# Kernel optimization log

Measured on AMD Instinct MI355X. Metric: run time of the kernel, lower is better.

The kernel has to match this reference:

```python
import jax, jax.numpy as jnp
import numpy as np

K = 8192
D = 512


def setup_inputs() -> dict:
    key = jax.random.key(0)
    k1, k2 = jax.random.split(key)
    x = jax.random.normal(k1, (32, 512, D), dtype=jnp.float32)
    # nn.Embedding weight init: uniform(-1/k, 1/k)
    codebook = jax.random.uniform(k2, (K, D), dtype=jnp.float32,
                                  minval=-1.0 / K, maxval=1.0 / K)
    return {"x": x, "codebook": codebook}


def reference(x, codebook):
    # flatten to [N, D]
    z_e = x.reshape(-1, x.shape[-1])
    # squared L2 distances: ||z||^2 - 2 z c^T + ||c||^2  -> [N, K]
    dists = (jnp.sum(z_e * z_e, axis=1, keepdims=True)
             - 2.0 * jnp.einsum('nd,kd->nk', z_e, codebook)
             + jnp.sum(codebook * codebook, axis=1)[None, :])
    indices = jnp.argmin(dists, axis=1)  # [N]
    z_q = codebook[indices]              # [N, D] gather
    # straight-through estimator: forward z_q, grad passes to z_e
    z_q_st = z_e + jax.lax.stop_gradient(z_q - z_e)
    # vq loss pulls codebook toward (detached) encoder outputs
    vq_loss = jnp.mean((z_q - jax.lax.stop_gradient(z_e)) ** 2)
    # commitment loss pulls encoder outputs toward (detached) codes
    commit_loss = jnp.mean((z_e - jax.lax.stop_gradient(z_q)) ** 2)
    z_q_out = z_q_st.reshape(x.shape)
    idx_out = indices.reshape(x.shape[:-1])
    return z_q_out, vq_loss, commit_loss, idx_out
```

## Files before the change

### kernel.cpp

```cpp
#include <hip/hip_runtime.h>

#define K_CODES 8192
#define D_DIM   512
#define N_ROWS  16384
#define NSPLIT  32
#define CAP     8
#define T2      2.0e-4f
#define LIST_CAP 32768

typedef __attribute__((ext_vector_type(8))) short bf16x8;
typedef __attribute__((ext_vector_type(4))) float f32x4;
typedef unsigned char uchar;
typedef unsigned short ushort;
typedef unsigned long long u64;

__device__ __forceinline__ unsigned fkey(float f) {
    unsigned b = __float_as_uint(f);
    return (b & 0x80000000u) ? ~b : (b | 0x80000000u);
}
__device__ __forceinline__ float finv(unsigned k) {
    return __uint_as_float((k & 0x80000000u) ? (k & 0x7fffffffu) : ~k);
}

__device__ __forceinline__ unsigned pk_bf16(float a, float b) {
    unsigned ua = __float_as_uint(a), ub = __float_as_uint(b);
    ua = (ua + 0x7fffu + ((ua >> 16) & 1u)) >> 16;
    ub = (ub + 0x7fffu + ((ub >> 16) & 1u)) & 0xffff0000u;
    return ua | ub;
}

__device__ __forceinline__ void gload_lds16(const void* g, void* l) {
    __builtin_amdgcn_global_load_lds(
        (const __attribute__((address_space(1))) unsigned int*)g,
        (__attribute__((address_space(3))) unsigned int*)l, 16, 0, 0);
}

__global__ void vq_prepass(const float* __restrict__ x, const float* __restrict__ cb,
                           unsigned* __restrict__ xb, unsigned* __restrict__ cbb,
                           float* __restrict__ sn, u64* __restrict__ keys,
                           int* __restrict__ count) {
    const int bid = blockIdx.x;
    const int t = threadIdx.x;
    if (bid < 6144) {
        const size_t gid = (size_t)bid * 256 + t;
        const size_t nx = (size_t)N_ROWS * D_DIM / 8;
        if (gid < nx) {
            const float4 f0 = ((const float4*)x)[gid * 2];
            const float4 f1 = ((const float4*)x)[gid * 2 + 1];
            ((uint4*)xb)[gid] = make_uint4(pk_bf16(f0.x, f0.y), pk_bf16(f0.z, f0.w),
                                           pk_bf16(f1.x, f1.y), pk_bf16(f1.z, f1.w));
        } else {
            const size_t g = gid - nx;
            const float4 f0 = ((const float4*)cb)[g * 2];
            const float4 f1 = ((const float4*)cb)[g * 2 + 1];
            ((uint4*)cbb)[g] = make_uint4(pk_bf16(f0.x, f0.y), pk_bf16(f0.z, f0.w),
                                          pk_bf16(f1.x, f1.y), pk_bf16(f1.z, f1.w));
        }
    } else {
        const int base = (bid - 6144) * 8;
        if (bid == 6144 && t == 0) *count = 0;
        if (t < 8) keys[base + t] = ~0ull;
        const int wave = t >> 6, lane = t & 63;
        const int row = base + wave * 2 + (lane >> 5);
        const int l = lane & 31, b = l >> 3, j = l & 7;
        const float* a = x + (size_t)row * D_DIM + b * 128 + j;
        float r = __fmul_rn(a[0], a[0]);
#pragma unroll
        for (int i = 1; i < 16; ++i) {
            const float v = a[i * 8];
            r = __fadd_rn(r, __fmul_rn(v, v));
        }
        r = __fadd_rn(r, __shfl_xor(r, 1));
        r = __fadd_rn(r, __shfl_xor(r, 2));
        r = __fadd_rn(r, __shfl_xor(r, 4));
        r = __fadd_rn(r, __shfl_xor(r, 8));
        r = __fadd_rn(r, __shfl_xor(r, 16));
        if (l == 0) sn[row] = r;
    }
}

__global__ __launch_bounds__(256)
void vq_sn(const float* __restrict__ x, float* __restrict__ sn,
           u64* __restrict__ keys, int* __restrict__ count) {
    const int t = threadIdx.x;
    const int base = blockIdx.x * 8;
    if (blockIdx.x == 0 && t == 0) *count = 0;
    if (t < 8) keys[base + t] = ~0ull;
    const int wave = t >> 6, lane = t & 63;
    const int row = base + wave * 2 + (lane >> 5);
    const int l = lane & 31, b = l >> 3, j = l & 7;
    const float* a = x + (size_t)row * D_DIM + b * 128 + j;
    float r = __fmul_rn(a[0], a[0]);
#pragma unroll
    for (int i = 1; i < 16; ++i) {
        const float v = a[i * 8];
        r = __fadd_rn(r, __fmul_rn(v, v));
    }
    r = __fadd_rn(r, __shfl_xor(r, 1));
    r = __fadd_rn(r, __shfl_xor(r, 2));
    r = __fadd_rn(r, __shfl_xor(r, 4));
    r = __fadd_rn(r, __shfl_xor(r, 8));
    r = __fadd_rn(r, __shfl_xor(r, 16));
    if (l == 0) sn[row] = r;
}

template<bool PRE>
__global__ __launch_bounds__(256, 2)
void vq_screen2(const float* __restrict__ x, const float* __restrict__ cb,
                const ushort* __restrict__ xb, const ushort* __restrict__ cbb,
                float* __restrict__ g_dmax, uchar* __restrict__ g_cnt,
                uchar* __restrict__ g_cand) {
    __shared__ ushort Ash[128 * 32];
    __shared__ ushort Bsh[256 * 32];
    __shared__ unsigned vkey[128];
    __shared__ int ccnt[128];
    __shared__ uchar clist[128][CAP];

    const int t    = threadIdx.x;
    const int w    = t >> 6, lane = t & 63;
    const int fr   = lane & 15;
    const int quad = lane >> 4;
    const int wr   = (w & 1) * 64;
    const int wc   = (w >> 1) * 128;
    const int row0  = blockIdx.y * 128;
    const int kbase = blockIdx.x * 256;

    if (t < 128) { vkey[t] = 0u; ccnt[t] = 0; }

    int aoff[4], boff[8];
#pragma unroll
    for (int i = 0; i < 4; ++i) {
        const int rw = wr + i * 16 + fr;
        aoff[i] = rw * 32 + ((quad ^ (rw >> 1)) & 3) * 8;
    }
#pragma unroll
    for (int j = 0; j < 8; ++j) {
        const int rw = wc + j * 16 + fr;
        boff[j] = rw * 32 + ((quad ^ (rw >> 1)) & 3) * 8;
    }

    f32x4 acc[4][8];
#pragma unroll
    for (int i = 0; i < 4; ++i)
#pragma unroll
        for (int j = 0; j < 8; ++j) acc[i][j] = (f32x4)0.0f;

    if (PRE) {
        const int la = lane >> 2;
        const int p  = lane & 3;
        const char* srcA0; const char* srcA1;
        const char* srcB0; const char* srcB1; const char* srcB2; const char* srcB3;
        ushort* dstA0; ushort* dstA1;
        ushort* dstB0; ushort* dstB1; ushort* dstB2; ushort* dstB3;
        {
            const int ia0 = w * 2 + 0, rA0 = ia0 * 16 + la;
            const int ia1 = w * 2 + 1, rA1 = ia1 * 16 + la;
            srcA0 = (const char*)xb + (size_t)(row0 + rA0) * 1024 + ((p ^ ((rA0 >> 1) & 3)) * 16);
            srcA1 = (const char*)xb + (size_t)(row0 + rA1) * 1024 + ((p ^ ((rA1 >> 1) & 3)) * 16);
            dstA0 = &Ash[ia0 * 512];
            dstA1 = &Ash[ia1 * 512];
            const int ib0 = w * 4 + 0, rB0 = ib0 * 16 + la;
            const int ib1 = w * 4 + 1, rB1 = ib1 * 16 + la;
            const int ib2 = w * 4 + 2, rB2 = ib2 * 16 + la;
            const int ib3 = w * 4 + 3, rB3 = ib3 * 16 + la;
            srcB0 = (const char*)cbb + (size_t)(kbase + rB0) * 1024 + ((p ^ ((rB0 >> 1) & 3)) * 16);
            srcB1 = (const char*)cbb + (size_t)(kbase + rB1) * 1024 + ((p ^ ((rB1 >> 1) & 3)) * 16);
            srcB2 = (const char*)cbb + (size_t)(kbase + rB2) * 1024 + ((p ^ ((rB2 >> 1) & 3)) * 16);
            srcB3 = (const char*)cbb + (size_t)(kbase + rB3) * 1024 + ((p ^ ((rB3 >> 1) & 3)) * 16);
            dstB0 = &Bsh[ib0 * 512];
            dstB1 = &Bsh[ib1 * 512];
            dstB2 = &Bsh[ib2 * 512];
            dstB3 = &Bsh[ib3 * 512];
        }
        for (int dc = 0; dc < 16; ++dc) {
            __syncthreads();
            gload_lds16(srcA0, dstA0);
            gload_lds16(srcA1, dstA1);
            gload_lds16(srcB0, dstB0);
            gload_lds16(srcB1, dstB1);
            gload_lds16(srcB2, dstB2);
            gload_lds16(srcB3, dstB3);
            srcA0 += 64; srcA1 += 64;
            srcB0 += 64; srcB1 += 64; srcB2 += 64; srcB3 += 64;
            __syncthreads();
            bf16x8 af[4], bfv[8];
#pragma unroll
            for (int i = 0; i < 4; ++i) af[i] = *(const bf16x8*)&Ash[aoff[i]];
#pragma unroll
            for (int j = 0; j < 8; ++j) bfv[j] = *(const bf16x8*)&Bsh[boff[j]];
#pragma unroll
            for (int i = 0; i < 4; ++i)
#pragma unroll
                for (int j = 0; j < 8; ++j)
                    acc[i][j] = __builtin_amdgcn_mfma_f32_16x16x32_bf16(af[i], bfv[j], acc[i][j], 0, 0, 0);
        }
    } else {
        const int r = t >> 1, h = t & 1;
        const int sA = (r >> 1) & 3;
        const int ca0 = (2 * h) ^ sA;
        ushort* awp0 = &Ash[r * 32 + ca0 * 8];
        ushort* awp1 = &Ash[r * 32 + (ca0 ^ 1) * 8];
        const int sB = (t >> 1) & 3;
        ushort* bwp0 = &Bsh[t * 32 + (0 ^ sB) * 8];
        ushort* bwp1 = &Bsh[t * 32 + (1 ^ sB) * 8];
        ushort* bwp2 = &Bsh[t * 32 + (2 ^ sB) * 8];
        ushort* bwp3 = &Bsh[t * 32 + (3 ^ sB) * 8];
        const char* gA = (const char*)(x  + (size_t)(row0 + r) * D_DIM + h * 16);
        const char* gB = (const char*)(cb + (size_t)(kbase + t) * D_DIM);
        for (int dc = 0; dc < 16; ++dc) {
            const float4* fa = (const float4*)(gA + dc * 128);
            float4 f0 = fa[0], f1 = fa[1], f2 = fa[2], f3 = fa[3];
            uint4 a0 = make_uint4(pk_bf16(f0.x, f0.y), pk_bf16(f0.z, f0.w),
                                  pk_bf16(f1.x, f1.y), pk_bf16(f1.z, f1.w));
            uint4 a1 = make_uint4(pk_bf16(f2.x, f2.y), pk_bf16(f2.z, f2.w),
                                  pk_bf16(f3.x, f3.y), pk_bf16(f3.z, f3.w));
            const float4* fb = (const float4*)(gB + dc * 128);
            float4 g0 = fb[0], g1 = fb[1], g2 = fb[2], g3 = fb[3];
            float4 g4 = fb[4], g5 = fb[5], g6 = fb[6], g7 = fb[7];
            uint4 b0 = make_uint4(pk_bf16(g0.x, g0.y), pk_bf16(g0.z, g0.w),
                                  pk_bf16(g1.x, g1.y), pk_bf16(g1.z, g1.w));
            uint4 b1 = make_uint4(pk_bf16(g2.x, g2.y), pk_bf16(g2.z, g2.w),
                                  pk_bf16(g3.x, g3.y), pk_bf16(g3.z, g3.w));
            uint4 b2 = make_uint4(pk_bf16(g4.x, g4.y), pk_bf16(g4.z, g4.w),
                                  pk_bf16(g5.x, g5.y), pk_bf16(g5.z, g5.w));
            uint4 b3 = make_uint4(pk_bf16(g6.x, g6.y), pk_bf16(g6.z, g6.w),
                                  pk_bf16(g7.x, g7.y), pk_bf16(g7.z, g7.w));
            __syncthreads();
            *(uint4*)awp0 = a0; *(uint4*)awp1 = a1;
            *(uint4*)bwp0 = b0; *(uint4*)bwp1 = b1;
            *(uint4*)bwp2 = b2; *(uint4*)bwp3 = b3;
            __syncthreads();
            bf16x8 af[4], bfv[8];
#pragma unroll
            for (int i = 0; i < 4; ++i) af[i] = *(const bf16x8*)&Ash[aoff[i]];
#pragma unroll
            for (int j = 0; j < 8; ++j) bfv[j] = *(const bf16x8*)&Bsh[boff[j]];
#pragma unroll
            for (int i = 0; i < 4; ++i)
#pragma unroll
                for (int j = 0; j < 8; ++j)
                    acc[i][j] = __builtin_amdgcn_mfma_f32_16x16x32_bf16(af[i], bfv[j], acc[i][j], 0, 0, 0);
        }
    }

    __syncthreads();
#pragma unroll
    for (int i = 0; i < 4; ++i)
#pragma unroll
        for (int rg = 0; rg < 4; ++rg) {
            float m = acc[i][0][rg];
#pragma unroll
            for (int j = 1; j < 8; ++j) m = fmaxf(m, acc[i][j][rg]);
            m = fmaxf(m, __shfl_xor(m, 1));
            m = fmaxf(m, __shfl_xor(m, 2));
            m = fmaxf(m, __shfl_xor(m, 4));
            m = fmaxf(m, __shfl_xor(m, 8));
            if (fr == 0) atomicMax(&vkey[wr + i * 16 + quad * 4 + rg], fkey(m));
        }
    __syncthreads();
#pragma unroll
    for (int i = 0; i < 4; ++i)
#pragma unroll
        for (int rg = 0; rg < 4; ++rg) {
            const int row = wr + i * 16 + quad * 4 + rg;
            const float thr = finv(vkey[row]) - T2;
#pragma unroll
            for (int j = 0; j < 8; ++j) {
                if (acc[i][j][rg] >= thr) {
                    int p = atomicAdd(&ccnt[row], 1);
                    if (p < CAP) clist[row][p] = (uchar)(wc + j * 16 + fr);
                }
            }
        }
    __syncthreads();
    if (t < 128) {
        const size_t o = (size_t)(row0 + t) * NSPLIT + blockIdx.x;
        g_dmax[o] = finv(vkey[t]);
        int c = ccnt[t];
        g_cnt[o] = (uchar)(c > 255 ? 255 : c);
        ((uint2*)g_cand)[o] = *(const uint2*)clist[t];
    }
}

__global__ __launch_bounds__(256)
void vq_build(const float* __restrict__ g_dmax, const uchar* __restrict__ g_cnt,
              const uchar* __restrict__ g_cand, int2* __restrict__ list,
              int* __restrict__ count, float* __restrict__ idx_f) {
    const int row = blockIdx.x * blockDim.x + threadIdx.x;
    const int lane = threadIdx.x & 63;
    const float* dm = g_dmax + (size_t)row * NSPLIT;
    float g = dm[0];
#pragma unroll
    for (int s = 1; s < NSPLIT; ++s) g = fmaxf(g, dm[s]);
    const float thr = g - T2;

    int tot = 0, first = -1;
    for (int s = 0; s < NSPLIT; ++s) {
        if (dm[s] < thr) continue;
        const size_t o = (size_t)row * NSPLIT + s;
        const int c = g_cnt[o];
        tot += (c > CAP) ? 256 : c;
        if (first < 0) first = s * 256 + g_cand[o * CAP];
    }
    idx_f[row] = (float)first;

    const int need = (tot > 1) ? tot : 0;
    int scan = need;
#pragma unroll
    for (int d = 1; d < 64; d <<= 1) {
        const int v = __shfl_up(scan, d, 64);
        if (lane >= d) scan += v;
    }
    const int wtot = __shfl(scan, 63, 64);
    int base = 0;
    if (lane == 63 && wtot > 0) base = atomicAdd(count, wtot);
    base = __shfl(base, 63, 64);
    if (need == 0) return;
    int pos = base + scan - need;

    for (int s = 0; s < NSPLIT; ++s) {
        if (dm[s] < thr) continue;
        const size_t o = (size_t)row * NSPLIT + s;
        const int c = g_cnt[o];
        if (c > CAP) {
            for (int u = 0; u < 256; ++u, ++pos)
                if (pos < LIST_CAP) list[pos] = make_int2(row, s * 256 + u);
        } else {
            for (int u = 0; u < c; ++u, ++pos)
                if (pos < LIST_CAP) list[pos] = make_int2(row, s * 256 + g_cand[o * CAP + u]);
        }
    }
}

__device__ __forceinline__ float np_einsum_dot(const float* __restrict__ a,
                                               const float* __restrict__ b) {
    float S0 = 0.f, S1 = 0.f, S2 = 0.f, S3 = 0.f;
    for (int i = 0; i < D_DIM; i += 16) {
        S0 = __fadd_rn(S0, __fmul_rn(a[i + 12], b[i + 12]));
        S1 = __fadd_rn(S1, __fmul_rn(a[i + 13], b[i + 13]));
        S2 = __fadd_rn(S2, __fmul_rn(a[i + 14], b[i + 14]));
        S3 = __fadd_rn(S3, __fmul_rn(a[i + 15], b[i + 15]));
        S0 = __fadd_rn(S0, __fmul_rn(a[i +  8], b[i +  8]));
        S1 = __fadd_rn(S1, __fmul_rn(a[i +  9], b[i +  9]));
        S2 = __fadd_rn(S2, __fmul_rn(a[i + 10], b[i + 10]));
        S3 = __fadd_rn(S3, __fmul_rn(a[i + 11], b[i + 11]));
        S0 = __fadd_rn(S0, __fmul_rn(a[i +  4], b[i +  4]));
        S1 = __fadd_rn(S1, __fmul_rn(a[i +  5], b[i +  5]));
        S2 = __fadd_rn(S2, __fmul_rn(a[i +  6], b[i +  6]));
        S3 = __fadd_rn(S3, __fmul_rn(a[i +  7], b[i +  7]));
        S0 = __fadd_rn(S0, __fmul_rn(a[i +  0], b[i +  0]));
        S1 = __fadd_rn(S1, __fmul_rn(a[i +  1], b[i +  1]));
        S2 = __fadd_rn(S2, __fmul_rn(a[i +  2], b[i +  2]));
        S3 = __fadd_rn(S3, __fmul_rn(a[i +  3], b[i +  3]));
    }
    return __fadd_rn(__fadd_rn(S0, S1), __fadd_rn(S2, S3));
}

__global__ __launch_bounds__(256)
void vq_replay(const float* __restrict__ x, const float* __restrict__ cb,
               const float* __restrict__ sn, const int2* __restrict__ list,
               const int* __restrict__ count, u64* __restrict__ keys) {
    const int i = blockIdx.x * blockDim.x + threadIdx.x;
    int n = *count; if (n > LIST_CAP) n = LIST_CAP;
    if (i >= n) return;
    const int2 e = list[i];
    const float* zr = x + (size_t)e.x * D_DIM;
    const float d = __fadd_rn(sn[e.x],
                              __fmul_rn(-2.0f, np_einsum_dot(zr, cb + (size_t)e.y * D_DIM)));
    const u64 key = ((u64)fkey(d) << 32) | (unsigned)e.y;
    atomicMin(&keys[e.x], key);
}

__global__ void vq_gather_kernel(const float* __restrict__ x,
                                 const float* __restrict__ cb,
                                 const u64* __restrict__ keys,
                                 float* __restrict__ idx_f,
                                 float* __restrict__ zq_out,
                                 double* __restrict__ psum) {
    const int row = blockIdx.x;
    const int t   = threadIdx.x;
    const u64 ky = keys[row];
    const int k = (ky != ~0ull) ? (int)(ky & 0xffffffffu) : (int)idx_f[row];
    const float4 c  = ((const float4*)(cb + (size_t)k   * D_DIM))[t];
    const float4 xv = ((const float4*)(x  + (size_t)row * D_DIM))[t];
    float4 o;
    o.x = __fadd_rn(xv.x, __fsub_rn(c.x, xv.x));
    o.y = __fadd_rn(xv.y, __fsub_rn(c.y, xv.y));
    o.z = __fadd_rn(xv.z, __fsub_rn(c.z, xv.z));
    o.w = __fadd_rn(xv.w, __fsub_rn(c.w, xv.w));
    ((float4*)(zq_out + (size_t)row * D_DIM))[t] = o;
    const double d0 = (double)c.x - (double)xv.x;
    const double d1 = (double)c.y - (double)xv.y;
    const double d2 = (double)c.z - (double)xv.z;
    const double d3 = (double)c.w - (double)xv.w;
    double s = d0 * d0 + d1 * d1 + d2 * d2 + d3 * d3;
#pragma unroll
    for (int off = 32; off > 0; off >>= 1) s += __shfl_xor(s, off, 64);
    __shared__ double red[2];
    if ((t & 63) == 0) red[t >> 6] = s;
    __syncthreads();
    if (t == 0) {
        psum[row] = red[0] + red[1];
        idx_f[row] = (float)k;
    }
}

__global__ void vq_finalize2(const double* __restrict__ psum,
                             float* __restrict__ losses) {
    __shared__ double red[4];
    const int t = threadIdx.x;
    double s = 0.0;
    for (int i = t; i < N_ROWS; i += 256) s += psum[i];
#pragma unroll
    for (int off = 32; off > 0; off >>= 1) s += __shfl_xor(s, off, 64);
    if ((t & 63) == 0) red[t >> 6] = s;
    __syncthreads();
    if (t == 0) {
        const double tot = red[0] + red[1] + red[2] + red[3];
        const float l = (float)(tot / (double)((size_t)N_ROWS * D_DIM));
        losses[0] = l;
        losses[1] = l;
    }
}

extern "C" void kernel_launch(void* const* d_in, const int* in_sizes, int n_in,
                              void* d_out, int out_size, void* d_ws, size_t ws_size,
                              hipStream_t stream) {
    const float* x  = (const float*)d_in[0];
    const float* cb = (const float*)d_in[1];
    float* out    = (float*)d_out;
    float* zq     = out;
    float* losses = out + (size_t)N_ROWS * D_DIM;
    float* idx_f  = losses + 2;
    char* ws = (char*)d_ws;

    const bool pre = (ws_size >= ((size_t)32 << 20));
    char* base = pre ? (ws + ((size_t)24 << 20)) : ws;

    float*  g_dmax = (float*)(base);
    uchar*  g_cnt  = (uchar*)(base + (2048u << 10));
    uchar*  g_cand = (uchar*)(base + (2560u << 10));
    float*  sn     = (float*)(base + (6656u << 10));
    u64*    keys   = (u64*)  (base + (6720u << 10));
    int2*   list   = (int2*) (base + (6848u << 10));
    int*    count  = (int*)  (base + (7104u << 10));
    double* psum   = (double*)(base + (7168u << 10));

    if (pre) {
        ushort* xb  = (ushort*)ws;
        ushort* cbb = (ushort*)(ws + ((size_t)16 << 20));
        hipLaunchKernelGGL(vq_prepass, dim3(8192), dim3(256), 0, stream,
                           x, cb, (unsigned*)xb, (unsigned*)cbb, sn, keys, count);
        hipLaunchKernelGGL((vq_screen2<true>), dim3(K_CODES / 256, N_ROWS / 128), dim3(256), 0, stream,
                           x, cb, xb, cbb, g_dmax, g_cnt, g_cand);
    } else {
        hipLaunchKernelGGL(vq_sn, dim3(N_ROWS / 8), dim3(256), 0, stream,
                           x, sn, keys, count);
        hipLaunchKernelGGL((vq_screen2<false>), dim3(K_CODES / 256, N_ROWS / 128), dim3(256), 0, stream,
                           x, cb, (const ushort*)nullptr, (const ushort*)nullptr,
                           g_dmax, g_cnt, g_cand);
    }
    hipLaunchKernelGGL(vq_build, dim3(N_ROWS / 256), dim3(256), 0, stream,
                       g_dmax, g_cnt, g_cand, list, count, idx_f);
    hipLaunchKernelGGL(vq_replay, dim3(LIST_CAP / 256), dim3(256), 0, stream,
                       x, cb, sn, list, count, keys);
    hipLaunchKernelGGL(vq_gather_kernel, dim3(N_ROWS), dim3(128), 0, stream,
                       x, cb, keys, idx_f, zq, psum);
    hipLaunchKernelGGL(vq_finalize2, dim3(1), dim3(256), 0, stream,
                       psum, losses);
}
```

Baseline: 384.7 us.

## Double-buffer LDS tiles in screening GEMM to overlap global loads with MFMA

```diff
diff --git a/kernel.cpp b/kernel.cpp
--- a/kernel.cpp
+++ b/kernel.cpp
@@ -110,8 +110,8 @@
                 const ushort* __restrict__ xb, const ushort* __restrict__ cbb,
                 float* __restrict__ g_dmax, uchar* __restrict__ g_cnt,
                 uchar* __restrict__ g_cand) {
-    __shared__ ushort Ash[128 * 32];
-    __shared__ ushort Bsh[256 * 32];
+    __shared__ ushort Ash[2][128 * 32];
+    __shared__ ushort Bsh[2][256 * 32];
     __shared__ unsigned vkey[128];
     __shared__ int ccnt[128];
     __shared__ uchar clist[128][CAP];
@@ -148,63 +148,63 @@
     if (PRE) {
         const int la = lane >> 2;
         const int p  = lane & 3;
-        const char* srcA0; const char* srcA1;
-        const char* srcB0; const char* srcB1; const char* srcB2; const char* srcB3;
-        ushort* dstA0; ushort* dstA1;
-        ushort* dstB0; ushort* dstB1; ushort* dstB2; ushort* dstB3;
-        {
-            const int ia0 = w * 2 + 0, rA0 = ia0 * 16 + la;
-            const int ia1 = w * 2 + 1, rA1 = ia1 * 16 + la;
-            srcA0 = (const char*)xb + (size_t)(row0 + rA0) * 1024 + ((p ^ ((rA0 >> 1) & 3)) * 16);
-            srcA1 = (const char*)xb + (size_t)(row0 + rA1) * 1024 + ((p ^ ((rA1 >> 1) & 3)) * 16);
-            dstA0 = &Ash[ia0 * 512];
-            dstA1 = &Ash[ia1 * 512];
-            const int ib0 = w * 4 + 0, rB0 = ib0 * 16 + la;
-            const int ib1 = w * 4 + 1, rB1 = ib1 * 16 + la;
-            const int ib2 = w * 4 + 2, rB2 = ib2 * 16 + la;
-            const int ib3 = w * 4 + 3, rB3 = ib3 * 16 + la;
-            srcB0 = (const char*)cbb + (size_t)(kbase + rB0) * 1024 + ((p ^ ((rB0 >> 1) & 3)) * 16);
-            srcB1 = (const char*)cbb + (size_t)(kbase + rB1) * 1024 + ((p ^ ((rB1 >> 1) & 3)) * 16);
-            srcB2 = (const char*)cbb + (size_t)(kbase + rB2) * 1024 + ((p ^ ((rB2 >> 1) & 3)) * 16);
-            srcB3 = (const char*)cbb + (size_t)(kbase + rB3) * 1024 + ((p ^ ((rB3 >> 1) & 3)) * 16);
-            dstB0 = &Bsh[ib0 * 512];
-            dstB1 = &Bsh[ib1 * 512];
-            dstB2 = &Bsh[ib2 * 512];
-            dstB3 = &Bsh[ib3 * 512];
-        }
+        const int ia0 = w * 2 + 0, rA0 = ia0 * 16 + la;
+        const int ia1 = w * 2 + 1, rA1 = ia1 * 16 + la;
+        const char* srcA0 = (const char*)xb + (size_t)(row0 + rA0) * 1024 + ((p ^ ((rA0 >> 1) & 3)) * 16);
+        const char* srcA1 = (const char*)xb + (size_t)(row0 + rA1) * 1024 + ((p ^ ((rA1 >> 1) & 3)) * 16);
+        const int dA0 = ia0 * 512, dA1 = ia1 * 512;
+        const int ib0 = w * 4 + 0, rB0 = ib0 * 16 + la;
+        const int ib1 = w * 4 + 1, rB1 = ib1 * 16 + la;
+        const int ib2 = w * 4 + 2, rB2 = ib2 * 16 + la;
+        const int ib3 = w * 4 + 3, rB3 = ib3 * 16 + la;
+        const char* srcB0 = (const char*)cbb + (size_t)(kbase + rB0) * 1024 + ((p ^ ((rB0 >> 1) & 3)) * 16);
+        const char* srcB1 = (const char*)cbb + (size_t)(kbase + rB1) * 1024 + ((p ^ ((rB1 >> 1) & 3)) * 16);
+        const char* srcB2 = (const char*)cbb + (size_t)(kbase + rB2) * 1024 + ((p ^ ((rB2 >> 1) & 3)) * 16);
+        const char* srcB3 = (const char*)cbb + (size_t)(kbase + rB3) * 1024 + ((p ^ ((rB3 >> 1) & 3)) * 16);
+
+#define STAGE6(buf, slab) do {                                     \
+        gload_lds16(srcA0 + (slab) * 64, &Ash[buf][dA0]);          \
+        gload_lds16(srcA1 + (slab) * 64, &Ash[buf][dA1]);          \
+        gload_lds16(srcB0 + (slab) * 64, &Bsh[buf][dB0]);          \
+        gload_lds16(srcB1 + (slab) * 64, &Bsh[buf][dB1]);          \
+        gload_lds16(srcB2 + (slab) * 64, &Bsh[buf][dB2]);          \
+        gload_lds16(srcB3 + (slab) * 64, &Bsh[buf][dB3]);          \
+    } while (0)
+        const int dB0 = ib0 * 512, dB1 = ib1 * 512, dB2 = ib2 * 512, dB3 = ib3 * 512;
+
+        STAGE6(0, 0);
+        asm volatile("s_waitcnt vmcnt(0)" ::: "memory");
+        __builtin_amdgcn_s_barrier();
+
+#pragma unroll 2
         for (int dc = 0; dc < 16; ++dc) {
-            __syncthreads();
-            gload_lds16(srcA0, dstA0);
-            gload_lds16(srcA1, dstA1);
-            gload_lds16(srcB0, dstB0);
-            gload_lds16(srcB1, dstB1);
-            gload_lds16(srcB2, dstB2);
-            gload_lds16(srcB3, dstB3);
-            srcA0 += 64; srcA1 += 64;
-            srcB0 += 64; srcB1 += 64; srcB2 += 64; srcB3 += 64;
-            __syncthreads();
+            const int cur = dc & 1;
+            if (dc < 15) STAGE6(cur ^ 1, dc + 1);
             bf16x8 af[4], bfv[8];
 #pragma unroll
-            for (int i = 0; i < 4; ++i) af[i] = *(const bf16x8*)&Ash[aoff[i]];
-#pragma unroll
-            for (int j = 0; j < 8; ++j) bfv[j] = *(const bf16x8*)&Bsh[boff[j]];
+            for (int i = 0; i < 4; ++i) af[i] = *(const bf16x8*)&Ash[cur][aoff[i]];
+#pragma unroll
+            for (int j = 0; j < 8; ++j) bfv[j] = *(const bf16x8*)&Bsh[cur][boff[j]];
 #pragma unroll
             for (int i = 0; i < 4; ++i)
 #pragma unroll
                 for (int j = 0; j < 8; ++j)
                     acc[i][j] = __builtin_amdgcn_mfma_f32_16x16x32_bf16(af[i], bfv[j], acc[i][j], 0, 0, 0);
-        }
+            asm volatile("s_waitcnt vmcnt(0)" ::: "memory");
+            __builtin_amdgcn_s_barrier();
+        }
+#undef STAGE6
     } else {
         const int r = t >> 1, h = t & 1;
         const int sA = (r >> 1) & 3;
         const int ca0 = (2 * h) ^ sA;
-        ushort* awp0 = &Ash[r * 32 + ca0 * 8];
-        ushort* awp1 = &Ash[r * 32 + (ca0 ^ 1) * 8];
+        ushort* awp0 = &Ash[0][r * 32 + ca0 * 8];
+        ushort* awp1 = &Ash[0][r * 32 + (ca0 ^ 1) * 8];
         const int sB = (t >> 1) & 3;
-        ushort* bwp0 = &Bsh[t * 32 + (0 ^ sB) * 8];
-        ushort* bwp1 = &Bsh[t * 32 + (1 ^ sB) * 8];
-        ushort* bwp2 = &Bsh[t * 32 + (2 ^ sB) * 8];
-        ushort* bwp3 = &Bsh[t * 32 + (3 ^ sB) * 8];
+        ushort* bwp0 = &Bsh[0][t * 32 + (0 ^ sB) * 8];
+        ushort* bwp1 = &Bsh[0][t * 32 + (1 ^ sB) * 8];
+        ushort* bwp2 = &Bsh[0][t * 32 + (2 ^ sB) * 8];
+        ushort* bwp3 = &Bsh[0][t * 32 + (3 ^ sB) * 8];
         const char* gA = (const char*)(x  + (size_t)(row0 + r) * D_DIM + h * 16);
         const char* gB = (const char*)(cb + (size_t)(kbase + t) * D_DIM);
         for (int dc = 0; dc < 16; ++dc) {
@@ -232,9 +232,9 @@
             __syncthreads();
             bf16x8 af[4], bfv[8];
 #pragma unroll
-            for (int i = 0; i < 4; ++i) af[i] = *(const bf16x8*)&Ash[aoff[i]];
-#pragma unroll
-            for (int j = 0; j < 8; ++j) bfv[j] = *(const bf16x8*)&Bsh[boff[j]];
+            for (int i = 0; i < 4; ++i) af[i] = *(const bf16x8*)&Ash[0][aoff[i]];
+#pragma unroll
+            for (int j = 0; j < 8; ++j) bfv[j] = *(const bf16x8*)&Bsh[0][boff[j]];
 #pragma unroll
             for (int i = 0; i < 4; ++i)
 #pragma unroll
```

Result: slower. 394.7 us (+2.6%).
